# Optimization experiments

Measured on AMD Instinct MI355X. Metric: run time of the kernel, lower is better.

Reference implementation:

```python
import jax, jax.numpy as jnp
import numpy as np

B, S, N, D = 32, 512, 64, 64


def setup_inputs() -> dict:
    key = jax.random.key(0)
    ks = jax.random.split(key, 6)
    return {
        "x": jax.random.normal(ks[0], (B, S, N, D), dtype=jnp.float32),
        "q_embed_weight": jax.random.normal(ks[1], (N, D), dtype=jnp.float32) * 0.02,
        "Wq_w": jax.random.normal(ks[2], (D, D), dtype=jnp.float32) * (1.0 / np.sqrt(D)),
        "Wq_b": jax.random.normal(ks[3], (D,), dtype=jnp.float32) * 0.02,
        "Wkv_w": jax.random.normal(ks[4], (2 * D, D), dtype=jnp.float32) * (1.0 / np.sqrt(D)),
        "Wkv_b": jax.random.normal(ks[5], (2 * D,), dtype=jnp.float32) * 0.02,
    }


def reference(x, q_embed_weight, Wq_w, Wq_b, Wkv_w, Wkv_b):
    d = x.shape[-1]
    # q = Wq(q_embed.weight): [n, d]
    q = q_embed_weight @ Wq_w.T + Wq_b
    # Wkv(x) -> [b, s, n, 2d]; chunk -> k is first half (v half is computed but unused, matching torch)
    kv = jnp.einsum('bsnd,ed->bsne', x, Wkv_w) + Wkv_b
    k = kv[..., :d]
    # prod: full contraction over n and d -> [b, s]
    prod = jnp.einsum('nd,bsnd->bs', q, k) / jnp.sqrt(jnp.asarray(d, x.dtype))
    attn = jax.nn.softmax(prod, axis=1)  # softmax over s
    # weighted sum over s with v = x (original overwrites v): [b, n, d]
    out = jnp.einsum('bs,bsnd->bnd', attn, x)
    return out
```

## Files before the change

kernel.cpp:

```cpp
#include <hip/hip_runtime.h>

#define B_   32
#define S_   512
#define N_   64
#define D_   64
#define ND_  4096
#define SCH  32
#define CH   16
#define R_   4

__global__ void qw_kernel(const float* __restrict__ qe, const float* __restrict__ Wq_w,
                          const float* __restrict__ Wq_b, const float* __restrict__ Wkv_w,
                          float* __restrict__ qw) {
    const int n = blockIdx.x;
    const int t = threadIdx.x;
    __shared__ float qrow[D_];
    float acc = Wq_b[t];
    const float* qen = qe + n * D_;
    const float* wqr = Wq_w + t * D_;
#pragma unroll 8
    for (int d = 0; d < D_; ++d) acc += qen[d] * wqr[d];
    qrow[t] = acc;
    __syncthreads();
    float s = 0.f;
#pragma unroll 8
    for (int e = 0; e < D_; ++e) s += qrow[e] * Wkv_w[e * D_ + t];
    qw[n * D_ + t] = s * 0.125f;
}

__global__ __launch_bounds__(256) void flash_partial(
    const float* __restrict__ x, const float* __restrict__ qw,
    float* __restrict__ po, float* __restrict__ pml) {
    const int blk  = blockIdx.x;
    const int b    = blk >> 5;
    const int c    = blk & (SCH - 1);
    const int t    = threadIdx.x;
    const int w    = t >> 6;
    const int lane = t & 63;
    const int s0   = c * CH;

    float4 qv[4];
#pragma unroll
    for (int k = 0; k < 4; ++k) qv[k] = *(const float4*)(qw + k * 1024 + t * 4);

    float o[4][4] = {{0.f, 0.f, 0.f, 0.f}};
    float m = -3.0e38f, l = 0.f;

    __shared__ float red[2][4][R_];

    const float* xb = x + (size_t)(b * S_ + s0) * ND_ + t * 4;

    for (int ph = 0; ph < CH / R_; ++ph) {
        const int par = ph & 1;
        const float* xp = xb + (size_t)(ph * R_) * ND_;

        float4 cur[R_][4];
#pragma unroll
        for (int r = 0; r < R_; ++r)
#pragma unroll
            for (int k = 0; k < 4; ++k)
                cur[r][k] = *(const float4*)(xp + (size_t)r * ND_ + k * 1024);

        float pd[R_];
#pragma unroll
        for (int r = 0; r < R_; ++r) {
            float s = 0.f;
#pragma unroll
            for (int k = 0; k < 4; ++k)
                s += cur[r][k].x * qv[k].x + cur[r][k].y * qv[k].y +
                     cur[r][k].z * qv[k].z + cur[r][k].w * qv[k].w;
            pd[r] = s;
        }

#pragma unroll
        for (int off = 32; off > 0; off >>= 1)
#pragma unroll
            for (int r = 0; r < R_; ++r)
                pd[r] += __shfl_xor(pd[r], off, 64);

        if (lane == 0) {
#pragma unroll
            for (int r = 0; r < R_; ++r) red[par][w][r] = pd[r];
        }
        __syncthreads();

        float p[R_];
#pragma unroll
        for (int r = 0; r < R_; ++r)
            p[r] = red[par][0][r] + red[par][1][r] + red[par][2][r] + red[par][3][r];

        float mb = fmaxf(fmaxf(p[0], p[1]), fmaxf(p[2], p[3]));
        const float mn = fmaxf(m, mb);
        const float sc = __expf(m - mn);
        float wt[R_], ws = 0.f;
#pragma unroll
        for (int r = 0; r < R_; ++r) { wt[r] = __expf(p[r] - mn); ws += wt[r]; }
        l = l * sc + ws;
#pragma unroll
        for (int k = 0; k < 4; ++k) {
#pragma unroll
            for (int j = 0; j < 4; ++j) {
                float* oe = &o[k][j];
                float acc = *oe * sc;
                acc += wt[0] * (&cur[0][k].x)[j];
                acc += wt[1] * (&cur[1][k].x)[j];
                acc += wt[2] * (&cur[2][k].x)[j];
                acc += wt[3] * (&cur[3][k].x)[j];
                *oe = acc;
            }
        }
        m = mn;
    }

    float* pob = po + (size_t)blk * ND_ + t * 4;
#pragma unroll
    for (int k = 0; k < 4; ++k) {
        float4 v = { o[k][0], o[k][1], o[k][2], o[k][3] };
        *(float4*)(pob + k * 1024) = v;
    }
    if (t == 0) { pml[blk * 2] = m; pml[blk * 2 + 1] = l; }
}

__global__ __launch_bounds__(256) void combine_kernel(
    const float* __restrict__ po, const float* __restrict__ pml,
    float* __restrict__ out) {
    const int b   = blockIdx.x >> 4;
    const int seg = blockIdx.x & 15;
    const int t   = threadIdx.x;
    const int idx = seg * 256 + t;
    __shared__ float sm[SCH], sl[SCH];
    if (t < SCH) {
        sm[t] = pml[(b * SCH + t) * 2];
        sl[t] = pml[(b * SCH + t) * 2 + 1];
    }
    __syncthreads();
    float M = -3.0e38f;
#pragma unroll
    for (int c = 0; c < SCH; ++c) M = fmaxf(M, sm[c]);
    float L = 0.f, acc = 0.f;
    for (int c = 0; c < SCH; ++c) {
        const float wc = __expf(sm[c] - M);
        L += wc * sl[c];
        acc += wc * po[(size_t)(b * SCH + c) * ND_ + idx];
    }
    out[(size_t)b * ND_ + idx] = acc / L;
}

extern "C" void kernel_launch(void* const* d_in, const int* in_sizes, int n_in,
                              void* d_out, int out_size, void* d_ws, size_t ws_size,
                              hipStream_t stream) {
    const float* x     = (const float*)d_in[0];
    const float* qe    = (const float*)d_in[1];
    const float* Wq_w  = (const float*)d_in[2];
    const float* Wq_b  = (const float*)d_in[3];
    const float* Wkv_w = (const float*)d_in[4];
    float* out = (float*)d_out;

    float* qw  = (float*)d_ws;
    float* pml = qw + ND_;
    float* po  = pml + (size_t)B_ * SCH * 2;

    qw_kernel<<<dim3(N_), dim3(D_), 0, stream>>>(qe, Wq_w, Wq_b, Wkv_w, qw);
    flash_partial<<<dim3(B_ * SCH), dim3(256), 0, stream>>>(x, qw, po, pml);
    combine_kernel<<<dim3(B_ * 16), dim3(256), 0, stream>>>(po, pml, out);
}
```

Before: 61.82 us.

## Give each wavefront its own rows in flash partial kernel, merge via shared memory

The flash partial kernel now assigns each 64-lane wavefront its own 8 sequence rows over the full 4096-element row, instead of splitting each row across four waves. This removes the per-phase cross-wave reduction and __syncthreads in the inner loop. The four per-wave online-softmax states are merged at the end through a 16KB shared buffer. Chunks are halved, so the combine kernel reads fewer partials. In exchange, registers per thread rise sharply (16 float4 for q, x and o each), and with fewer blocks (512) occupancy and latency hiding may suffer.

Result: faster. 57.65 us (-6.7%).

```diff
diff --git a/kernel.cpp b/kernel.cpp
--- a/kernel.cpp
+++ b/kernel.cpp
@@ -2,123 +2,121 @@
 
 #define B_   32
 #define S_   512
-#define N_   64
-#define D_   64
 #define ND_  4096
-#define SCH  32
-#define CH   16
-#define R_   4
+#define SCH  16
+#define CH   32
+#define RW   8
 
 __global__ void qw_kernel(const float* __restrict__ qe, const float* __restrict__ Wq_w,
                           const float* __restrict__ Wq_b, const float* __restrict__ Wkv_w,
                           float* __restrict__ qw) {
     const int n = blockIdx.x;
     const int t = threadIdx.x;
-    __shared__ float qrow[D_];
+    __shared__ float qrow[64];
     float acc = Wq_b[t];
-    const float* qen = qe + n * D_;
-    const float* wqr = Wq_w + t * D_;
+    const float* qen = qe + n * 64;
+    const float* wqr = Wq_w + t * 64;
 #pragma unroll 8
-    for (int d = 0; d < D_; ++d) acc += qen[d] * wqr[d];
+    for (int d = 0; d < 64; ++d) acc += qen[d] * wqr[d];
     qrow[t] = acc;
     __syncthreads();
     float s = 0.f;
 #pragma unroll 8
-    for (int e = 0; e < D_; ++e) s += qrow[e] * Wkv_w[e * D_ + t];
-    qw[n * D_ + t] = s * 0.125f;
+    for (int e = 0; e < 64; ++e) s += qrow[e] * Wkv_w[e * 64 + t];
+    qw[n * 64 + t] = s * 0.125f;
 }
 
-__global__ __launch_bounds__(256) void flash_partial(
+__global__ __launch_bounds__(256, 2) void flash_partial(
     const float* __restrict__ x, const float* __restrict__ qw,
     float* __restrict__ po, float* __restrict__ pml) {
-    const int blk  = blockIdx.x;
-    const int b    = blk >> 5;
-    const int c    = blk & (SCH - 1);
-    const int t    = threadIdx.x;
-    const int w    = t >> 6;
-    const int lane = t & 63;
-    const int s0   = c * CH;
+    const int blk = blockIdx.x;
+    const int b   = blk >> 4;
+    const int c   = blk & (SCH - 1);
+    const int t   = threadIdx.x;
+    const int w   = t >> 6;
+    const int l   = t & 63;
 
-    float4 qv[4];
+    const float4* qw4 = (const float4*)qw;
+    float4 qv[16];
 #pragma unroll
-    for (int k = 0; k < 4; ++k) qv[k] = *(const float4*)(qw + k * 1024 + t * 4);
+    for (int j = 0; j < 16; ++j) qv[j] = qw4[j * 64 + l];
 
-    float o[4][4] = {{0.f, 0.f, 0.f, 0.f}};
-    float m = -3.0e38f, l = 0.f;
+    float4 o[16];
+#pragma unroll
+    for (int j = 0; j < 16; ++j) o[j] = make_float4(0.f, 0.f, 0.f, 0.f);
+    float m = -3.0e38f, lsum = 0.f;
 
-    __shared__ float red[2][4][R_];
+    const int s0 = c * CH + w * RW;
+    const float4* xb = (const float4*)(x) + (size_t)(b * S_ + s0) * 1024;
 
-    const float* xb = x + (size_t)(b * S_ + s0) * ND_ + t * 4;
+    for (int r = 0; r < RW; ++r) {
+        const float4* xr = xb + (size_t)r * 1024;
+        float4 cur[16];
+#pragma unroll
+        for (int j = 0; j < 16; ++j) cur[j] = xr[j * 64 + l];
 
-    for (int ph = 0; ph < CH / R_; ++ph) {
-        const int par = ph & 1;
-        const float* xp = xb + (size_t)(ph * R_) * ND_;
-
-        float4 cur[R_][4];
+        float pd = 0.f;
 #pragma unroll
-        for (int r = 0; r < R_; ++r)
-#pragma unroll
-            for (int k = 0; k < 4; ++k)
-                cur[r][k] = *(const float4*)(xp + (size_t)r * ND_ + k * 1024);
-
-        float pd[R_];
-#pragma unroll
-        for (int r = 0; r < R_; ++r) {
-            float s = 0.f;
-#pragma unroll
-            for (int k = 0; k < 4; ++k)
-                s += cur[r][k].x * qv[k].x + cur[r][k].y * qv[k].y +
-                     cur[r][k].z * qv[k].z + cur[r][k].w * qv[k].w;
-            pd[r] = s;
-        }
-
+        for (int j = 0; j < 16; ++j)
+            pd += cur[j].x * qv[j].x + cur[j].y * qv[j].y +
+                  cur[j].z * qv[j].z + cur[j].w * qv[j].w;
 #pragma unroll
         for (int off = 32; off > 0; off >>= 1)
+            pd += __shfl_xor(pd, off, 64);
+
+        const float mn = fmaxf(m, pd);
+        const float sc = __expf(m - mn);
+        const float wt = __expf(pd - mn);
+        lsum = lsum * sc + wt;
 #pragma unroll
-            for (int r = 0; r < R_; ++r)
-                pd[r] += __shfl_xor(pd[r], off, 64);
-
-        if (lane == 0) {
-#pragma unroll
-            for (int r = 0; r < R_; ++r) red[par][w][r] = pd[r];
-        }
-        __syncthreads();
-
-        float p[R_];
-#pragma unroll
-        for (int r = 0; r < R_; ++r)
-            p[r] = red[par][0][r] + red[par][1][r] + red[par][2][r] + red[par][3][r];
-
-        float mb = fmaxf(fmaxf(p[0], p[1]), fmaxf(p[2], p[3]));
-        const float mn = fmaxf(m, mb);
-        const float sc = __expf(m - mn);
-        float wt[R_], ws = 0.f;
-#pragma unroll
-        for (int r = 0; r < R_; ++r) { wt[r] = __expf(p[r] - mn); ws += wt[r]; }
-        l = l * sc + ws;
-#pragma unroll
-        for (int k = 0; k < 4; ++k) {
-#pragma unroll
-            for (int j = 0; j < 4; ++j) {
-                float* oe = &o[k][j];
-                float acc = *oe * sc;
-                acc += wt[0] * (&cur[0][k].x)[j];
-                acc += wt[1] * (&cur[1][k].x)[j];
-                acc += wt[2] * (&cur[2][k].x)[j];
-                acc += wt[3] * (&cur[3][k].x)[j];
-                *oe = acc;
-            }
+        for (int j = 0; j < 16; ++j) {
+            o[j].x = o[j].x * sc + wt * cur[j].x;
+            o[j].y = o[j].y * sc + wt * cur[j].y;
+            o[j].z = o[j].z * sc + wt * cur[j].z;
+            o[j].w = o[j].w * sc + wt * cur[j].w;
         }
         m = mn;
     }
 
-    float* pob = po + (size_t)blk * ND_ + t * 4;
+    __shared__ float  sml[4][2];
+    __shared__ float4 obuf[1024];
+    if (l == 0) { sml[w][0] = m; sml[w][1] = lsum; }
+    __syncthreads();
+    const float M = fmaxf(fmaxf(sml[0][0], sml[1][0]), fmaxf(sml[2][0], sml[3][0]));
+    float L = 0.f;
 #pragma unroll
-    for (int k = 0; k < 4; ++k) {
-        float4 v = { o[k][0], o[k][1], o[k][2], o[k][3] };
-        *(float4*)(pob + k * 1024) = v;
+    for (int ww = 0; ww < 4; ++ww) L += __expf(sml[ww][0] - M) * sml[ww][1];
+    const float wk = __expf(sml[w][0] - M);
+
+    if (w == 0) {
+#pragma unroll
+        for (int j = 0; j < 16; ++j) {
+            float4 v = { wk * o[j].x, wk * o[j].y, wk * o[j].z, wk * o[j].w };
+            obuf[j * 64 + l] = v;
+        }
     }
-    if (t == 0) { pml[blk * 2] = m; pml[blk * 2 + 1] = l; }
+    __syncthreads();
+#pragma unroll
+    for (int ww = 1; ww < 4; ++ww) {
+        if (w == ww) {
+#pragma unroll
+            for (int j = 0; j < 16; ++j) {
+                float4 v = obuf[j * 64 + l];
+                v.x += wk * o[j].x; v.y += wk * o[j].y;
+                v.z += wk * o[j].z; v.w += wk * o[j].w;
+                obuf[j * 64 + l] = v;
+            }
+        }
+        __syncthreads();
+    }
+
+    float4* pob = (float4*)(po) + (size_t)blk * 1024;
+#pragma unroll
+    for (int jj = 0; jj < 4; ++jj) {
+        const int j = w * 4 + jj;
+        pob[j * 64 + l] = obuf[j * 64 + l];
+    }
+    if (t == 0) { pml[blk * 2] = M; pml[blk * 2 + 1] = L; }
 }
 
 __global__ __launch_bounds__(256) void combine_kernel(
@@ -138,6 +136,7 @@
 #pragma unroll
     for (int c = 0; c < SCH; ++c) M = fmaxf(M, sm[c]);
     float L = 0.f, acc = 0.f;
+#pragma unroll
     for (int c = 0; c < SCH; ++c) {
         const float wc = __expf(sm[c] - M);
         L += wc * sl[c];
@@ -160,7 +159,7 @@
     float* pml = qw + ND_;
     float* po  = pml + (size_t)B_ * SCH * 2;
 
-    qw_kernel<<<dim3(N_), dim3(D_), 0, stream>>>(qe, Wq_w, Wq_b, Wkv_w, qw);
+    qw_kernel<<<dim3(64), dim3(64), 0, stream>>>(qe, Wq_w, Wq_b, Wkv_w, qw);
     flash_partial<<<dim3(B_ * SCH), dim3(256), 0, stream>>>(x, qw, po, pml);
     combine_kernel<<<dim3(B_ * 16), dim3(256), 0, stream>>>(po, pml, out);
 }
```
